# Kernel optimization log

Hardware: AMD Instinct MI355X
Metric: run time of the kernel (lower is better)

## Reference

```python
import jax, jax.numpy as jnp
import numpy as np
import math

EMBED_DIM = 2048
NUM_HEADS = 16
HEAD_DIM = EMBED_DIM // NUM_HEADS
SCALE = 1.0 / math.sqrt(HEAD_DIM)

# ALiBi slopes for power-of-2 num_heads: base = 2**(-2**(-(log2(H)-3))), slopes = base**i, i=1..H
_BASE = 2.0 ** (-2.0 ** (-(math.log2(NUM_HEADS) - 3)))
ALIBI_SLOPES = np.array([_BASE ** i for i in range(1, NUM_HEADS + 1)], dtype=np.float32)


def setup_inputs() -> dict:
    key = jax.random.key(0)
    ks = jax.random.split(key, 7)
    B, L, D, R_KV, R_Q = 2, 2048, EMBED_DIM, 512, 1536
    std = 0.02
    return {
        "hidden_states": jax.random.normal(ks[0], (B, L, D), jnp.float32),
        "Wq_down": jax.random.normal(ks[1], (R_Q, D), jnp.float32) * std,
        "Wq_up": jax.random.normal(ks[2], (NUM_HEADS * HEAD_DIM, R_Q), jnp.float32) * std,
        "Wkv_down": jax.random.normal(ks[3], (R_KV, D), jnp.float32) * std,
        "k_up": jax.random.normal(ks[4], (NUM_HEADS, R_KV, HEAD_DIM), jnp.float32) * std,
        "v_up": jax.random.normal(ks[5], (NUM_HEADS, R_KV, HEAD_DIM), jnp.float32) * std,
        "Wo": jax.random.normal(ks[6], (D, D), jnp.float32) * std,
    }


def reference(hidden_states, Wq_down, Wq_up, Wkv_down, k_up, v_up, Wo):
    B, L, D = hidden_states.shape
    # Query: low-rank down/up projection
    q = (hidden_states @ Wq_down.T) @ Wq_up.T            # [B, L, H*d]
    q = q.reshape(B, L, NUM_HEADS, HEAD_DIM).transpose(0, 2, 1, 3)  # [B, H, L, d]
    # Shared compressed latent KV
    c = hidden_states @ Wkv_down.T                        # [B, L, r]
    k = jnp.einsum('bsr,hrd->bhsd', c, k_up)              # [B, H, L, d]
    v = jnp.einsum('bsr,hrd->bhsd', c, v_up)
    scores = jnp.einsum('bhqd,bhkd->bhqk', q, k) * SCALE  # [B, H, L, L]
    # ALiBi bias: -slope_h * |i - j|
    pos = jnp.arange(L)
    dist = jnp.abs(pos[:, None] - pos[None, :]).astype(jnp.float32)
    slopes = jnp.asarray(ALIBI_SLOPES)
    scores = scores - slopes[None, :, None, None] * dist[None, None, :, :]
    # Causal mask
    causal = pos[:, None] >= pos[None, :]
    scores = jnp.where(causal[None, None], scores, -jnp.inf)
    attn = jax.nn.softmax(scores.astype(jnp.float32), axis=-1).astype(scores.dtype)
    out = jnp.einsum('bhqk,bhkd->bhqd', attn, v)          # [B, H, L, d]
    out = out.transpose(0, 2, 1, 3).reshape(B, L, D)
    return out @ Wo.T
```

## Files before the change

kernel.cpp:

```cpp
#include <hip/hip_runtime.h>
#include <math.h>


typedef __bf16 bf16;
typedef __bf16 bf16x8 __attribute__((ext_vector_type(8)));
typedef __bf16 bf16x4 __attribute__((ext_vector_type(4)));
typedef float f32x4 __attribute__((ext_vector_type(4)));

#define AS1 __attribute__((address_space(1)))
#define AS3 __attribute__((address_space(3)))

#define ATTN_BLOCKS 792
#define COMB_BLOCKS 168

struct ATables {
  int tbl[ATTN_BLOCKS * 2];
  int grp[COMB_BLOCKS * 4];
};

constexpr ATables make_tables() {
  ATables T{};
  int WH[16] = {22,32,45,64,90,128,181,256,362,512,724,1024,1448,2048,2896,4096};
  int nc = 0, np = 0, ng = 0;
  for (int qt = 15; qt >= 0; --qt)
    for (int h = 15; h >= 0; --h)
      for (int b = 0; b < 2; ++b) {
        int q0 = qt * 128, nkv = 2 * qt + 2;
        int dlo = q0 - WH[h];
        int kv_lo = dlo > 0 ? (dlo >> 6) : 0;
        int span = nkv - kv_lo;
        int nch = (span + 7) >> 3;
        int base = b | (h << 1) | (qt << 5);
        if (nch == 1) {
          T.tbl[2 * nc] = base | (kv_lo << 9) | (span << 16);
          T.tbl[2 * nc + 1] = -1;
          ++nc;
        } else {
          T.grp[4 * ng] = base; T.grp[4 * ng + 1] = np; T.grp[4 * ng + 2] = nch;
          ++ng;
          for (int c = 0; c < nch; ++c) {
            int cs = kv_lo + c * 8;
            int cl = nkv - cs; if (cl > 8) cl = 8;
            T.tbl[2 * nc] = base | (cs << 9) | (cl << 16);
            T.tbl[2 * nc + 1] = np;
            ++nc; ++np;
          }
        }
      }
  return T;
}

__device__ const ATables g_tab = make_tables();

__device__ __forceinline__ void g2l16(const void* g, void* l) {
  __builtin_amdgcn_global_load_lds((const AS1 void*)g, (AS3 void*)l, 16, 0, 0);
}

__device__ __forceinline__ void cvt_seg(const float* __restrict__ in,
                                        bf16* __restrict__ out, int n4) {
  int i = blockIdx.x * 256 + threadIdx.x;
  const int stride = gridDim.x * 256;
  for (; i < n4; i += stride) {
    float4 v = ((const float4*)in)[i];
    bf16x4 o;
    o[0] = (bf16)v.x; o[1] = (bf16)v.y; o[2] = (bf16)v.z; o[3] = (bf16)v.w;
    ((bf16x4*)out)[i] = o;
  }
}

__global__ __launch_bounds__(256) void cvt_f32_bf16(
    const float* __restrict__ in, bf16* __restrict__ out, int n4) {
  cvt_seg(in, out, n4);
}

__global__ __launch_bounds__(256) void cvt3_f32_bf16(
    const float* __restrict__ s0, bf16* __restrict__ d0, int n0,
    const float* __restrict__ s1, bf16* __restrict__ d1, int n1,
    const float* __restrict__ s2, bf16* __restrict__ d2, int n2) {
  cvt_seg(s0, d0, n0);
  cvt_seg(s1, d1, n1);
  cvt_seg(s2, d2, n2);
}

__global__ __launch_bounds__(256) void transpose_cvt(
    const float* __restrict__ in, bf16* __restrict__ out, int R, int D)
{
  __shared__ bf16 tile[64][72];
  const long long base = (long long)blockIdx.z * R * D;
  const int r0 = blockIdx.y * 64, c0 = blockIdx.x * 64;
  const int t = threadIdx.x;
#pragma unroll
  for (int i = 0; i < 4; ++i) {
    int c = i * 256 + t;
    int rr = c >> 4, cc = (c & 15) << 2;
    float4 v = *(const float4*)&in[base + (long long)(r0 + rr) * D + c0 + cc];
    tile[rr][cc + 0] = (bf16)v.x;
    tile[rr][cc + 1] = (bf16)v.y;
    tile[rr][cc + 2] = (bf16)v.z;
    tile[rr][cc + 3] = (bf16)v.w;
  }
  __syncthreads();
#pragma unroll
  for (int i = 0; i < 2; ++i) {
    int c = i * 256 + t;
    int rr = c >> 3, cc = (c & 7) << 3;
    bf16x8 v;
#pragma unroll
    for (int j = 0; j < 8; ++j) v[j] = tile[cc + j][rr];
    *(bf16x8*)&out[base + (long long)(c0 + rr) * R + r0 + cc] = v;
  }
}

template <typename CT>
__global__ __launch_bounds__(256) void gemm_nt(
    const bf16* __restrict__ A, const bf16* __restrict__ B, CT* __restrict__ C,
    int lda, int ldb, int ldc, int K, long long sA, long long sB, long long sC)
{
  A += (long long)blockIdx.z * sA;
  B += (long long)blockIdx.z * sB;
  C += (long long)blockIdx.z * sC;

  __shared__ bf16 As[128][32];
  __shared__ bf16 Bs[128][32];

  const int t = threadIdx.x;
  const int lane = t & 63, wave = t >> 6;
  const int wm = (wave >> 1) * 64, wn = (wave & 1) * 64;
  const int m0 = blockIdx.y * 128, n0 = blockIdx.x * 128;
  const int r16 = lane & 15, q8 = (lane >> 4) * 8;

  f32x4 acc[4][4] = {};

  for (int k0 = 0; k0 < K; k0 += 32) {
    __syncthreads();
#pragma unroll
    for (int r = 0; r < 2; ++r) {
      int c = r * 256 + t;
      int row = c >> 2, col = (c & 3) << 3;
      g2l16(A + (long long)(m0 + row) * lda + (k0 + col), &As[row][col]);
      g2l16(B + (long long)(n0 + row) * ldb + (k0 + col), &Bs[row][col]);
    }
    __syncthreads();

    bf16x8 af[4], bfr[4];
#pragma unroll
    for (int i = 0; i < 4; ++i) af[i]  = *(const bf16x8*)&As[wm + i * 16 + r16][q8];
#pragma unroll
    for (int i = 0; i < 4; ++i) bfr[i] = *(const bf16x8*)&Bs[wn + i * 16 + r16][q8];
#pragma unroll
    for (int mi = 0; mi < 4; ++mi)
#pragma unroll
      for (int ni = 0; ni < 4; ++ni)
        acc[mi][ni] = __builtin_amdgcn_mfma_f32_16x16x32_bf16(af[mi], bfr[ni], acc[mi][ni], 0, 0, 0);
  }

  const int quad = lane >> 4;
#pragma unroll
  for (int mi = 0; mi < 4; ++mi)
#pragma unroll
    for (int ni = 0; ni < 4; ++ni)
#pragma unroll
      for (int r = 0; r < 4; ++r) {
        int mm = m0 + wm + mi * 16 + quad * 4 + r;
        int nn = n0 + wn + ni * 16 + r16;
        C[(long long)mm * ldc + nn] = (CT)acc[mi][ni][r];
      }
}

__global__ __launch_bounds__(256) void attn_kernel(
    const bf16* __restrict__ Q, const bf16* __restrict__ Kh,
    const bf16* __restrict__ VT, bf16* __restrict__ O,
    float* __restrict__ ml, bf16* __restrict__ parts)
{
  const int L = 2048, HD = 128, D = 2048;
  const int meta = g_tab.tbl[2 * blockIdx.x];
  const int part = g_tab.tbl[2 * blockIdx.x + 1];
  const int b = meta & 1, h = (meta >> 1) & 15, qt = (meta >> 5) & 15;
  const int cs = (meta >> 9) & 127, cl = (meta >> 16) & 15;
  const int q0 = qt * 128, nkv = 2 * qt + 2;
  const int cend = cs + cl;
  const int mraw = nkv - 2 > cs ? nkv - 2 : cs;
  const int mstart = mraw < cend ? mraw : cend;

  const int t = threadIdx.x, wave = t >> 6, lane = t & 63;
  const int col = lane & 15, quad = lane >> 4;
  const float slope = exp2f(-0.5f * (float)(h + 1));
  const float slope16 = slope * 16.0f;
  const float scale = 0.08838834764831845f;

  __shared__ bf16 Ksf[2][64 * 128];
  __shared__ bf16 Vsf[2][128 * 64];
  __shared__ bf16 Psf[128 * 64];

  const long long qrow0 = (long long)(b * L + q0 + wave * 32);
  const long long kbase = (long long)(h * 4096 + b * L) * HD;
  const long long vbase = (long long)(h * HD) * 4096 + b * L;

  auto stage = [&](int buf, int itile) {
    const int kv0 = itile << 6;
#pragma unroll
    for (int i = 0; i < 4; ++i) {
      int P = i * 256 + t;
      {
        int rr = P >> 4, cc = ((P & 15) ^ (rr & 15)) << 3;
        g2l16(Kh + kbase + (long long)(kv0 + rr) * HD + cc, &Ksf[buf][P * 8]);
      }
      {
        int rr = P >> 3, cc = ((P & 7) ^ (rr & 7)) << 3;
        g2l16(VT + vbase + (long long)rr * 4096 + kv0 + cc, &Vsf[buf][P * 8]);
      }
    }
  };

  bf16x8 qf[2][4];
#pragma unroll
  for (int mi = 0; mi < 2; ++mi)
#pragma unroll
    for (int ks = 0; ks < 4; ++ks)
      qf[mi][ks] = *(const bf16x8*)&Q[(qrow0 + mi * 16 + col) * D + h * HD + ks * 32 + quad * 8];

  f32x4 o_acc[2][8] = {};
  float m_i[2][4], l_i[2][4];
#pragma unroll
  for (int mi = 0; mi < 2; ++mi)
#pragma unroll
    for (int r = 0; r < 4; ++r) { m_i[mi][r] = -1e30f; l_i[mi][r] = 0.f; }

  stage(0, cs);

  for (int it = cs; it < cend; ++it) {
    const int cur = (it - cs) & 1;
    const int kv0 = it << 6;
    const bool masked = (it >= mstart);

    __syncthreads();
    if (it + 1 < cend) stage(cur ^ 1, it + 1);

    f32x4 s_acc[2][4] = {};
#pragma unroll
    for (int ks = 0; ks < 4; ++ks) {
      bf16x8 kf[4];
#pragma unroll
      for (int ni = 0; ni < 4; ++ni)
        kf[ni] = *(const bf16x8*)&Ksf[cur][(ni * 16 + col) * 128 +
                                          (((ks * 4 + quad) ^ col) << 3)];
#pragma unroll
      for (int mi = 0; mi < 2; ++mi)
#pragma unroll
        for (int ni = 0; ni < 4; ++ni)
          s_acc[mi][ni] = __builtin_amdgcn_mfma_f32_16x16x32_bf16(
              qf[mi][ks], kf[ni], s_acc[mi][ni], 0, 0, 0);
    }

#pragma unroll
    for (int mi = 0; mi < 2; ++mi) {
#pragma unroll
      for (int r = 0; r < 4; ++r) {
        const int rowq = wave * 32 + mi * 16 + quad * 4 + r;
        const int qg = q0 + rowq;
        const float sb = slope * (float)(qg - kv0 - col);
        float sv[4];
#pragma unroll
        for (int ni = 0; ni < 4; ++ni)
          sv[ni] = fmaf(s_acc[mi][ni][r], scale, (float)ni * slope16 - sb);
        if (masked) {
#pragma unroll
          for (int ni = 0; ni < 4; ++ni)
            if (kv0 + ni * 16 + col > qg) sv[ni] = -1e30f;
        }
        float rm = fmaxf(fmaxf(sv[0], sv[1]), fmaxf(sv[2], sv[3]));
#pragma unroll
        for (int off = 1; off < 16; off <<= 1)
          rm = fmaxf(rm, __shfl_xor(rm, off, 64));
        const float mold = m_i[mi][r];
        float mnew = fmaxf(mold, rm);
        if (masked) mnew = fmaxf(mnew, -1e20f);
        const float alpha = __expf(mold - mnew);
        float ps = 0.f;
#pragma unroll
        for (int ni = 0; ni < 4; ++ni) {
          float pv = __expf(sv[ni] - mnew);
          ps += pv;
          Psf[rowq * 64 + ((((ni * 2) + (col >> 3)) ^ (rowq & 7)) << 3) +
              (col & 7)] = (bf16)pv;
        }
        l_i[mi][r] = fmaf(alpha, l_i[mi][r], ps);
        m_i[mi][r] = mnew;
#pragma unroll
        for (int di = 0; di < 8; ++di) o_acc[mi][di][r] *= alpha;
      }
    }

#pragma unroll
    for (int kstep = 0; kstep < 2; ++kstep) {
      bf16x8 pf[2];
#pragma unroll
      for (int mi = 0; mi < 2; ++mi)
        pf[mi] = *(const bf16x8*)&Psf[(wave * 32 + mi * 16 + col) * 64 +
                                      (((kstep * 4 + quad) ^ (col & 7)) << 3)];
#pragma unroll
      for (int di = 0; di < 8; ++di) {
        bf16x8 vf = *(const bf16x8*)&Vsf[cur][(di * 16 + col) * 64 +
                                             (((kstep * 4 + quad) ^ (col & 7)) << 3)];
#pragma unroll
        for (int mi = 0; mi < 2; ++mi)
          o_acc[mi][di] = __builtin_amdgcn_mfma_f32_16x16x32_bf16(
              pf[mi], vf, o_acc[mi][di], 0, 0, 0);
      }
    }
  }

  if (part < 0) {
#pragma unroll
    for (int mi = 0; mi < 2; ++mi)
#pragma unroll
      for (int r = 0; r < 4; ++r) {
        float lt = l_i[mi][r];
#pragma unroll
        for (int off = 1; off < 16; off <<= 1)
          lt += __shfl_xor(lt, off, 64);
        float rl = 1.0f / lt;
        long long qg = qrow0 + mi * 16 + quad * 4 + r;
#pragma unroll
        for (int di = 0; di < 8; ++di)
          O[qg * D + h * HD + di * 16 + col] = (bf16)(o_acc[mi][di][r] * rl);
      }
  } else {
    bf16* pb = parts + (long long)part * 16384;
    float* mlp = ml + (long long)part * 256;
#pragma unroll
    for (int mi = 0; mi < 2; ++mi)
#pragma unroll
      for (int r = 0; r < 4; ++r) {
        float lt = l_i[mi][r];
#pragma unroll
        for (int off = 1; off < 16; off <<= 1)
          lt += __shfl_xor(lt, off, 64);
        int rowq = wave * 32 + mi * 16 + quad * 4 + r;
        if (col == 0) { mlp[rowq] = m_i[mi][r]; mlp[128 + rowq] = lt; }
#pragma unroll
        for (int di = 0; di < 8; ++di)
          pb[rowq * 128 + di * 16 + col] = (bf16)o_acc[mi][di][r];
      }
  }
}

__global__ __launch_bounds__(256) void attn_combine(
    const float* __restrict__ ml, const bf16* __restrict__ parts,
    bf16* __restrict__ O)
{
  const int meta = g_tab.grp[4 * blockIdx.x];
  const int first = g_tab.grp[4 * blockIdx.x + 1];
  const int n = g_tab.grp[4 * blockIdx.x + 2];
  const int b = meta & 1, h = (meta >> 1) & 15, qt = (meta >> 5) & 15;
  const int t = threadIdx.x;
  const int row = t >> 1, cg = t & 1;

  float M = -1e30f;
  for (int c = 0; c < n; ++c) M = fmaxf(M, ml[(long long)(first + c) * 256 + row]);

  float acc[64];
#pragma unroll
  for (int j = 0; j < 64; ++j) acc[j] = 0.f;
  float den = 0.f;
  for (int c = 0; c < n; ++c) {
    const float* mlc = ml + (long long)(first + c) * 256;
    float w = __expf(mlc[row] - M);
    den = fmaf(w, mlc[128 + row], den);
    const bf16* p = parts + (long long)(first + c) * 16384 + row * 128 + cg * 64;
#pragma unroll
    for (int j8 = 0; j8 < 8; ++j8) {
      bf16x8 v = ((const bf16x8*)p)[j8];
#pragma unroll
      for (int k = 0; k < 8; ++k) acc[j8 * 8 + k] = fmaf(w, (float)v[k], acc[j8 * 8 + k]);
    }
  }
  float rd = 1.0f / den;
  long long qg = (long long)b * 2048 + qt * 128 + row;
  bf16* o = O + qg * 2048 + h * 128 + cg * 64;
#pragma unroll
  for (int j8 = 0; j8 < 8; ++j8) {
    bf16x8 v;
#pragma unroll
    for (int k = 0; k < 8; ++k) v[k] = (bf16)(acc[j8 * 8 + k] * rd);
    ((bf16x8*)o)[j8] = v;
  }
}

extern "C" void kernel_launch(void* const* d_in, const int* in_sizes, int n_in,
                              void* d_out, int out_size, void* d_ws, size_t ws_size,
                              hipStream_t stream) {
  (void)in_sizes; (void)n_in; (void)out_size; (void)ws_size;
  const float* hs  = (const float*)d_in[0];
  const float* Wqd = (const float*)d_in[1];
  const float* Wqu = (const float*)d_in[2];
  const float* Wkv = (const float*)d_in[3];
  const float* kup = (const float*)d_in[4];
  const float* vup = (const float*)d_in[5];
  const float* Wo  = (const float*)d_in[6];
  float* out = (float*)d_out;

  char* ws = (char*)d_ws;
  bf16* hsb  = (bf16*)ws; ws += (size_t)4096 * 2048 * 2;
  bf16* Wdcb = (bf16*)ws; ws += (size_t)2048 * 2048 * 2;
  bf16* Wqub = (bf16*)ws; ws += (size_t)2048 * 1536 * 2;
  bf16* kupT = (bf16*)ws; ws += (size_t)16 * 128 * 512 * 2;
  bf16* vupT = (bf16*)ws; ws += (size_t)16 * 128 * 512 * 2;
  bf16* XC   = (bf16*)ws; ws += (size_t)4096 * 2048 * 2;
  bf16* Qb   = (bf16*)ws; ws += (size_t)4096 * 2048 * 2;
  bf16* Kb   = (bf16*)ws; ws += (size_t)16 * 4096 * 128 * 2;
  bf16* VTb  = (bf16*)ws; ws += (size_t)16 * 128 * 4096 * 2;
  bf16* Cl   = XC + 1536;
  bf16* Ob   = hsb;
  bf16* Wob  = XC;

  float* mld   = (float*)Wdcb;
  bf16*  parts = (bf16*)(mld + 448 * 256);

  cvt_f32_bf16<<<1024, 256, 0, stream>>>(hs, hsb, 4096 * 2048 / 4);
  cvt3_f32_bf16<<<1024, 256, 0, stream>>>(
      Wqd, Wdcb, 1536 * 2048 / 4,
      Wkv, Wdcb + (size_t)1536 * 2048, 512 * 2048 / 4,
      Wqu, Wqub, 2048 * 1536 / 4);
  transpose_cvt<<<dim3(2, 8, 16), 256, 0, stream>>>(kup, kupT, 512, 128);
  transpose_cvt<<<dim3(2, 8, 16), 256, 0, stream>>>(vup, vupT, 512, 128);

  gemm_nt<bf16><<<dim3(16, 32, 1), 256, 0, stream>>>(hsb, Wdcb, XC,
                                                     2048, 2048, 2048, 2048, 0, 0, 0);
  gemm_nt<bf16><<<dim3(16, 32, 1), 256, 0, stream>>>(XC, Wqub, Qb,
                                                     2048, 1536, 2048, 1536, 0, 0, 0);
  gemm_nt<bf16><<<dim3(1, 32, 16), 256, 0, stream>>>(Cl, kupT, Kb,
                                                     2048, 512, 128, 512,
                                                     0, 128 * 512, (long long)4096 * 128);
  gemm_nt<bf16><<<dim3(32, 1, 16), 256, 0, stream>>>(vupT, Cl, VTb,
                                                     512, 2048, 4096, 512,
                                                     128 * 512, 0, (long long)128 * 4096);
  cvt_f32_bf16<<<512, 256, 0, stream>>>(Wo, Wob, 2048 * 2048 / 4);
  attn_kernel<<<dim3(ATTN_BLOCKS, 1, 1), 256, 0, stream>>>(Qb, Kb, VTb, Ob, mld, parts);
  attn_combine<<<dim3(COMB_BLOCKS, 1, 1), 256, 0, stream>>>(mld, parts, Ob);
  gemm_nt<float><<<dim3(16, 32, 1), 256, 0, stream>>>(Ob, Wob, out,
                                                      2048, 2048, 2048, 2048, 0, 0, 0);
}
```

Measured before the change: 438.5 us.

## Use exp2 softmax, lazy rescaling, reverse KV order, and MFMA priority hints

The softmax moves to base-2 exponent space by folding log2(e) into the scale and ALiBi slope, and the combine kernel weights switch to exp2 to match. KV tiles are now visited from the diagonal backward, so the largest scores, which are closest under ALiBi, come first. With that order, an online rescale (row-max shuffle reduction, alpha multiply of the accumulator) is done only when some row's max grows by more than a threshold. The kernel also adds setprio around the MFMA phases and a launch-bounds occupancy hint of 2. The lazy rescale keeps a stale max and risks overflow or precision loss if the threshold is crossed in unexpected ways, and the occupancy hint may cause register spills.

```diff
diff --git a/kernel.cpp b/kernel.cpp
--- a/kernel.cpp
+++ b/kernel.cpp
@@ -1,6 +1,5 @@
 #include <hip/hip_runtime.h>
 #include <math.h>
-
 
 typedef __bf16 bf16;
 typedef __bf16 bf16x8 __attribute__((ext_vector_type(8)));
@@ -167,7 +166,7 @@
       }
 }
 
-__global__ __launch_bounds__(256) void attn_kernel(
+__global__ __launch_bounds__(256, 2) void attn_kernel(
     const bf16* __restrict__ Q, const bf16* __restrict__ Kh,
     const bf16* __restrict__ VT, bf16* __restrict__ O,
     float* __restrict__ ml, bf16* __restrict__ parts)
@@ -184,9 +183,10 @@
 
   const int t = threadIdx.x, wave = t >> 6, lane = t & 63;
   const int col = lane & 15, quad = lane >> 4;
-  const float slope = exp2f(-0.5f * (float)(h + 1));
-  const float slope16 = slope * 16.0f;
-  const float scale = 0.08838834764831845f;
+  const float LOG2E = 1.44269504f;
+  const float slope2 = exp2f(-0.5f * (float)(h + 1)) * LOG2E;
+  const float slope16 = slope2 * 16.0f;
+  const float scale2 = 0.08838834764831845f * LOG2E;
 
   __shared__ bf16 Ksf[2][64 * 128];
   __shared__ bf16 Vsf[2][128 * 64];
@@ -226,17 +226,18 @@
 #pragma unroll
     for (int r = 0; r < 4; ++r) { m_i[mi][r] = -1e30f; l_i[mi][r] = 0.f; }
 
-  stage(0, cs);
-
-  for (int it = cs; it < cend; ++it) {
-    const int cur = (it - cs) & 1;
+  stage(0, cend - 1);
+
+  for (int it = cend - 1; it >= cs; --it) {
+    const int cur = (cend - 1 - it) & 1;
     const int kv0 = it << 6;
     const bool masked = (it >= mstart);
 
     __syncthreads();
-    if (it + 1 < cend) stage(cur ^ 1, it + 1);
+    if (it > cs) stage(cur ^ 1, it - 1);
 
     f32x4 s_acc[2][4] = {};
+    __builtin_amdgcn_s_setprio(1);
 #pragma unroll
     for (int ks = 0; ks < 4; ++ks) {
       bf16x8 kf[4];
@@ -251,46 +252,78 @@
           s_acc[mi][ni] = __builtin_amdgcn_mfma_f32_16x16x32_bf16(
               qf[mi][ks], kf[ni], s_acc[mi][ni], 0, 0, 0);
     }
-
-#pragma unroll
-    for (int mi = 0; mi < 2; ++mi) {
+    __builtin_amdgcn_s_setprio(0);
+
+    float sv[2][4][4];
+    float grow = -1e30f;
+#pragma unroll
+    for (int mi = 0; mi < 2; ++mi)
 #pragma unroll
       for (int r = 0; r < 4; ++r) {
         const int rowq = wave * 32 + mi * 16 + quad * 4 + r;
         const int qg = q0 + rowq;
-        const float sb = slope * (float)(qg - kv0 - col);
-        float sv[4];
+        const float sb = slope2 * (float)(qg - kv0 - col);
 #pragma unroll
         for (int ni = 0; ni < 4; ++ni)
-          sv[ni] = fmaf(s_acc[mi][ni][r], scale, (float)ni * slope16 - sb);
+          sv[mi][r][ni] = fmaf(s_acc[mi][ni][r], scale2, (float)ni * slope16 - sb);
         if (masked) {
 #pragma unroll
           for (int ni = 0; ni < 4; ++ni)
-            if (kv0 + ni * 16 + col > qg) sv[ni] = -1e30f;
+            if (kv0 + ni * 16 + col > qg) sv[mi][r][ni] = -1e30f;
         }
-        float rm = fmaxf(fmaxf(sv[0], sv[1]), fmaxf(sv[2], sv[3]));
-#pragma unroll
-        for (int off = 1; off < 16; off <<= 1)
-          rm = fmaxf(rm, __shfl_xor(rm, off, 64));
-        const float mold = m_i[mi][r];
-        float mnew = fmaxf(mold, rm);
-        if (masked) mnew = fmaxf(mnew, -1e20f);
-        const float alpha = __expf(mold - mnew);
-        float ps = 0.f;
-#pragma unroll
-        for (int ni = 0; ni < 4; ++ni) {
-          float pv = __expf(sv[ni] - mnew);
-          ps += pv;
-          Psf[rowq * 64 + ((((ni * 2) + (col >> 3)) ^ (rowq & 7)) << 3) +
-              (col & 7)] = (bf16)pv;
+        float rm = fmaxf(fmaxf(sv[mi][r][0], sv[mi][r][1]),
+                         fmaxf(sv[mi][r][2], sv[mi][r][3]));
+        grow = fmaxf(grow, rm - m_i[mi][r]);
+      }
+
+    if (!__any(grow > 20.0f)) {
+#pragma unroll
+      for (int mi = 0; mi < 2; ++mi)
+#pragma unroll
+        for (int r = 0; r < 4; ++r) {
+          const int rowq = wave * 32 + mi * 16 + quad * 4 + r;
+          const float mref = m_i[mi][r];
+          float ps = 0.f;
+#pragma unroll
+          for (int ni = 0; ni < 4; ++ni) {
+            float pv = exp2f(sv[mi][r][ni] - mref);
+            ps += pv;
+            Psf[rowq * 64 + ((((ni * 2) + (col >> 3)) ^ (rowq & 7)) << 3) +
+                (col & 7)] = (bf16)pv;
+          }
+          l_i[mi][r] += ps;
         }
-        l_i[mi][r] = fmaf(alpha, l_i[mi][r], ps);
-        m_i[mi][r] = mnew;
-#pragma unroll
-        for (int di = 0; di < 8; ++di) o_acc[mi][di][r] *= alpha;
-      }
-    }
-
+    } else {
+#pragma unroll
+      for (int mi = 0; mi < 2; ++mi)
+#pragma unroll
+        for (int r = 0; r < 4; ++r) {
+          const int rowq = wave * 32 + mi * 16 + quad * 4 + r;
+          float rm = fmaxf(fmaxf(sv[mi][r][0], sv[mi][r][1]),
+                           fmaxf(sv[mi][r][2], sv[mi][r][3]));
+#pragma unroll
+          for (int off = 1; off < 16; off <<= 1)
+            rm = fmaxf(rm, __shfl_xor(rm, off, 64));
+          const float mold = m_i[mi][r];
+          float mnew = fmaxf(mold, rm);
+          if (masked) mnew = fmaxf(mnew, -1e20f);
+          const float alpha = exp2f(mold - mnew);
+          float ps = 0.f;
+#pragma unroll
+          for (int ni = 0; ni < 4; ++ni) {
+            float pv = exp2f(sv[mi][r][ni] - mnew);
+            ps += pv;
+            Psf[rowq * 64 + ((((ni * 2) + (col >> 3)) ^ (rowq & 7)) << 3) +
+                (col & 7)] = (bf16)pv;
+          }
+          l_i[mi][r] = fmaf(alpha, l_i[mi][r], ps);
+          m_i[mi][r] = mnew;
+#pragma unroll
+          for (int di = 0; di < 8; ++di) o_acc[mi][di][r] *= alpha;
+        }
+    }
+
+    __builtin_amdgcn_s_setprio(1);
 #pragma unroll
     for (int kstep = 0; kstep < 2; ++kstep) {
       bf16x8 pf[2];
@@ -308,6 +341,7 @@
               pf[mi], vf, o_acc[mi][di], 0, 0, 0);
       }
     }
+    __builtin_amdgcn_s_setprio(0);
   }
 
   if (part < 0) {
@@ -365,7 +399,7 @@
   float den = 0.f;
   for (int c = 0; c < n; ++c) {
     const float* mlc = ml + (long long)(first + c) * 256;
-    float w = __expf(mlc[row] - M);
+    float w = exp2f(mlc[row] - M);
     den = fmaf(w, mlc[128 + row], den);
     const bf16* p = parts + (long long)(first + c) * 16384 + row * 128 + cg * 64;
 #pragma unroll
```

After: 503.3 us. 14.8% more time.
